# Performance work log

Hardware: AMD Instinct MI355X
Metric: run time of the kernel (lower is better)

Reference implementation:

```python
import jax, jax.numpy as jnp
import numpy as np

B, N, C, K, T = 64, 1024, 256, 512, 64
D_THRESH = 0.5
POWER_ITERS = 20


def _pdist(x):
    # x: [..., K, 3] -> pairwise euclidean distances [..., K, K]
    n = jnp.sum(x * x, axis=-1)
    sq = n[..., :, None] + n[..., None, :] - 2.0 * jnp.einsum('...kc,...lc->...kl', x, x)
    return jnp.sqrt(jnp.maximum(sq, 0.0) + 1e-12)


def _forward(rt, rt_centroids, rt_cls_attn, shift_and_scale, W_in, b_in, W1, b1, W2, b2,
             num_rt, anc_idx, pos_idx, neg_idx):
    valid = jnp.arange(N)[None, :] < num_rt[:, None]                      # [B,N]
    # Normalize.batch_unnormalize: pts * scale + shift on valid tokens
    shift = shift_and_scale[:, None, :3]
    scale = shift_and_scale[:, None, 3:4]
    cent = jnp.where(valid[..., None], rt_centroids * scale + shift, rt_centroids)
    attn = jnp.where(valid, rt_cls_attn, -1e9)
    _, top_idx = jax.lax.top_k(attn, K)                                   # [B,K]
    cent_k = jnp.take_along_axis(cent, top_idx[..., None], axis=1)        # [B,K,3]
    rt_k = jnp.take_along_axis(rt, top_idx[..., None], axis=1)            # [B,K,C]
    # SGV padding mask [T,2,K,K]: rows masked by anchor count, cols by pos/neg counts
    n_eff = jnp.minimum(num_rt, K)
    r = jnp.arange(K)
    row_mask = r[None, :] < n_eff[anc_idx][:, None]                       # [T,K]
    col_mask = jnp.stack([r[None, :] < n_eff[pos_idx][:, None],
                          r[None, :] < n_eff[neg_idx][:, None]], axis=1)  # [T,2,K]
    mask = row_mask[:, None, :, None] & col_mask[:, :, None, :]           # [T,2,K,K]
    # input_linear on anchor / neighbour relay tokens
    anc_f = rt_k[anc_idx] @ W_in + b_in                                   # [T,K,C]
    nn_f = jnp.stack([rt_k[pos_idx], rt_k[neg_idx]], axis=1) @ W_in + b_in  # [T,2,K,C]
    anc_c = cent_k[anc_idx]                                               # [T,K,3]
    nn_c = jnp.stack([cent_k[pos_idx], cent_k[neg_idx]], axis=1)          # [T,2,K,3]
    # feature-space nearest-neighbour correspondences anc -> nn (SpectralGV style)
    fd = (jnp.sum(anc_f ** 2, -1)[:, None, :, None]
          + jnp.sum(nn_f ** 2, -1)[:, :, None, :]
          - 2.0 * jnp.einsum('tkc,tnlc->tnkl', anc_f, nn_f))              # [T,2,K,K]
    corr = jnp.argmin(fd, axis=-1)                                        # [T,2,K]
    q_c = jnp.take_along_axis(nn_c, corr[..., None], axis=2)              # [T,2,K,3]
    q_f = jnp.take_along_axis(nn_f, corr[..., None], axis=2)              # [T,2,K,C]
    # correspondence confidence from feature cosine similarity
    cos = jnp.sum(anc_f[:, None] * q_f, -1) / (
        jnp.linalg.norm(anc_f, axis=-1)[:, None] * jnp.linalg.norm(q_f, axis=-1) + 1e-8)
    s = jax.nn.relu(cos)                                                  # [T,2,K]
    # threshold-masked geometric consistency adjacency
    d_p = _pdist(anc_c)[:, None]                                          # [T,1,K,K]
    d_q = _pdist(q_c)                                                     # [T,2,K,K]
    geo = (jnp.abs(d_p - d_q) < D_THRESH) & mask & (~jnp.eye(K, dtype=bool))
    A = geo.astype(jnp.float32) * s[..., :, None] * s[..., None, :]       # [T,2,K,K]
    # leading eigenvector via power iteration (A is entrywise nonnegative)
    v = jnp.full((T, 2, K), 1.0 / np.sqrt(K), dtype=jnp.float32)
    for _ in range(POWER_ITERS):
        w = jnp.einsum('tnkl,tnl->tnk', A, v)
        v = w / (jnp.linalg.norm(w, axis=-1, keepdims=True) + 1e-8)
    eig = -jnp.sort(-v, axis=-1)                                          # sort_eigvec, descending
    h = jax.nn.relu(eig @ W1 + b1)
    scores = jax.nn.sigmoid(h @ W2 + b2)                                  # [T,2,1]
    targets = jnp.zeros_like(scores).at[:, 0].set(1.0)
    return scores, targets


def setup_inputs() -> dict:
    key = jax.random.key(0)
    ks = jax.random.split(key, 12)
    return {
        'rt': jax.random.normal(ks[0], (B, N, C), jnp.float32),
        'rt_centroids': jax.random.normal(ks[1], (B, N, 3), jnp.float32),
        'rt_cls_attn': jax.random.uniform(ks[2], (B, N), jnp.float32),
        'shift_and_scale': jax.random.uniform(ks[3], (B, 4), jnp.float32),
        'num_rt': jax.random.randint(ks[4], (B,), 128, N, jnp.int32),
        'anc_idx': jax.random.randint(ks[5], (T,), 0, B, jnp.int32),
        'pos_idx': jax.random.randint(ks[6], (T,), 0, B, jnp.int32),
        'neg_idx': jax.random.randint(ks[7], (T,), 0, B, jnp.int32),
        'W_in': jax.random.normal(ks[8], (C, C), jnp.float32) / np.sqrt(C),
        'b_in': jnp.zeros((C,), jnp.float32),
        'W1': jax.random.normal(ks[9], (K, K), jnp.float32) / np.sqrt(K),
        'b1': jnp.zeros((K,), jnp.float32),
        'W2': jax.random.normal(ks[10], (K, 1), jnp.float32) / np.sqrt(K),
        'b2': jnp.zeros((1,), jnp.float32),
    }


def reference(rt, rt_centroids, rt_cls_attn, shift_and_scale, num_rt, anc_idx, pos_idx, neg_idx,
              W_in, b_in, W1, b1, W2, b2):
    return _forward(rt, rt_centroids, rt_cls_attn, shift_and_scale, W_in, b_in, W1, b1, W2, b2,
                    num_rt, anc_idx, pos_idx, neg_idx)
```

## Files before the change

kernel.cpp:

```cpp
#include <hip/hip_runtime.h>
#include <cstddef>

#define BB 64
#define NN 1024
#define CC 256
#define KK 512
#define TT 64
#define NPAIR 128

typedef _Float16 h8 __attribute__((ext_vector_type(8)));
typedef _Float16 h4 __attribute__((ext_vector_type(4)));
typedef float f4 __attribute__((ext_vector_type(4)));

typedef __attribute__((address_space(1))) const void GV;
typedef __attribute__((address_space(3))) void LV;
#define GLDS16(g, s) __builtin_amdgcn_global_load_lds((GV*)(const void*)(g), (LV*)(void*)(s), 16, 0, 0)


__global__ __launch_bounds__(256) void wtrans_kernel(
    const float* __restrict__ Win, _Float16* __restrict__ wth, _Float16* __restrict__ wtl)
{
    __shared__ float t[64][65];
    const int k0 = blockIdx.x * 64, n0 = blockIdx.y * 64;
    const int tid = threadIdx.x;
    const int c = tid & 63, r0 = tid >> 6;
    for (int r = r0; r < 64; r += 4)
        t[r][c] = Win[(size_t)(k0 + r) * CC + n0 + c];
    __syncthreads();
    for (int r = r0; r < 64; r += 4) {
        float x = t[c][r];
        _Float16 h = (_Float16)x;
        size_t o = (size_t)(n0 + r) * CC + k0 + c;
        wth[o] = h;
        wtl[o] = (_Float16)(x - (float)h);
    }
}

__global__ __launch_bounds__(512) void sel_kernel(
    const float* __restrict__ attn, const float* __restrict__ cents,
    const float* __restrict__ sas, const int* __restrict__ num_rt,
    int* __restrict__ topidx, int* __restrict__ neff, float* __restrict__ centk)
{
    __shared__ unsigned long long keys[1024];
    const int b = blockIdx.x, tid = threadIdx.x;
    const int nr = num_rt[b];
    for (int i = tid; i < 1024; i += 512) {
        float a = (i < nr) ? attn[b * NN + i] : -1e9f;
        unsigned u = __float_as_uint(a);
        u = (u & 0x80000000u) ? ~u : (u | 0x80000000u);
        keys[i] = ((unsigned long long)u << 32) | (unsigned)(0xFFFFFFFFu - (unsigned)i);
    }
    __syncthreads();
    for (int k = 2; k <= 1024; k <<= 1) {
        for (int j = k >> 1; j > 0; j >>= 1) {
            int i = ((tid & ~(j - 1)) << 1) | (tid & (j - 1));
            int p = i | j;
            unsigned long long a = keys[i], c = keys[p];
            bool up = (i & k) == 0;
            if (up ? (a < c) : (a > c)) { keys[i] = c; keys[p] = a; }
            __syncthreads();
        }
    }
    {
        unsigned long long key = keys[tid];
        int idx = (int)(~(unsigned)key);
        float x = cents[(b * NN + idx) * 3 + 0];
        float y = cents[(b * NN + idx) * 3 + 1];
        float z = cents[(b * NN + idx) * 3 + 2];
        if (idx < nr) {
            float sc = sas[b * 4 + 3];
            x = x * sc + sas[b * 4 + 0];
            y = y * sc + sas[b * 4 + 1];
            z = z * sc + sas[b * 4 + 2];
        }
        float nc = x * x + y * y + z * z;
        ((float4*)centk)[b * KK + tid] = make_float4(x, y, z, nc);
        topidx[b * KK + tid] = idx;
    }
    if (tid == 0) neff[b] = (nr < KK) ? nr : KK;
}

__global__ __launch_bounds__(256) void feat_mfma(
    const float* __restrict__ rt, const int* __restrict__ topidx,
    const _Float16* __restrict__ wth, const _Float16* __restrict__ wtl,
    const float* __restrict__ bin,
    _Float16* __restrict__ feath, _Float16* __restrict__ featl)
{
    const int mtile = blockIdx.x, nt = blockIdx.y;
    __shared__ _Float16 Ah[128][32], Al[128][32], Bh[128][32], Bl[128][32];
    __shared__ int tix[128];
    const int tid = threadIdx.x;
    const int w = tid >> 6, lane = tid & 63;
    const int quad = lane >> 4, l16 = lane & 15;
    const int wm = (w >> 1) * 64, wl = (w & 1) * 64;
    const int b = mtile >> 2;
    if (tid < 128) tix[tid] = topidx[mtile * 128 + tid];
    __syncthreads();
    const int arow_i = tid >> 1;
    const int aseg = (tid & 1) * 16;
    const int asw = (arow_i >> 1) & 3;
    const float* arow = rt + ((size_t)b * NN + tix[arow_i]) * CC + aseg;
    _Float16* bsh = (w < 2) ? &Bh[0][0] : &Bl[0][0];
    const _Float16* bplane = (w < 2) ? wth : wtl;
    const int rowi = lane >> 2, chunk = lane & 3;
    const int ssw = (rowi >> 1) & 3;
    const int rsw = (l16 >> 1) & 3;

    f4 acc[4][4];
    #pragma unroll
    for (int i = 0; i < 4; i++)
        #pragma unroll
        for (int j = 0; j < 4; j++)
            acc[i][j] = (f4){0.f, 0.f, 0.f, 0.f};

    for (int k0 = 0; k0 < CC; k0 += 32) {
        __syncthreads();
        #pragma unroll
        for (int jj = 0; jj < 4; jj++) {
            int j = (w & 1) * 4 + jj;
            int row = j * 16 + rowi;
            GLDS16(bplane + (size_t)(nt * 128 + row) * CC + k0 + (chunk ^ ssw) * 8, bsh + j * 512);
        }
        {
            const float4* src = (const float4*)(arow + k0);
            #pragma unroll
            for (int c = 0; c < 2; c++) {
                float4 p = src[2 * c], q2 = src[2 * c + 1];
                float xv[8] = {p.x, p.y, p.z, p.w, q2.x, q2.y, q2.z, q2.w};
                h8 hv, lv;
                #pragma unroll
                for (int j = 0; j < 8; j++) {
                    _Float16 h = (_Float16)xv[j];
                    hv[j] = h;
                    lv[j] = (_Float16)(xv[j] - (float)h);
                }
                int ci = ((tid & 1) * 2 + c) ^ asw;
                *(h8*)&Ah[arow_i][ci * 8] = hv;
                *(h8*)&Al[arow_i][ci * 8] = lv;
            }
        }
        __syncthreads();
        h8 afh[4], afl[4], bfh[4], bfl[4];
        #pragma unroll
        for (int i = 0; i < 4; i++) {
            int ra = wm + i * 16 + l16;
            int rb = wl + i * 16 + l16;
            int qa = (quad ^ rsw) * 8;
            afh[i] = *(const h8*)&Ah[ra][qa];
            afl[i] = *(const h8*)&Al[ra][qa];
            bfh[i] = *(const h8*)&Bh[rb][qa];
            bfl[i] = *(const h8*)&Bl[rb][qa];
        }
        #pragma unroll
        for (int i = 0; i < 4; i++)
            #pragma unroll
            for (int j = 0; j < 4; j++) {
                acc[i][j] = __builtin_amdgcn_mfma_f32_16x16x32_f16(afh[i], bfh[j], acc[i][j], 0, 0, 0);
                acc[i][j] = __builtin_amdgcn_mfma_f32_16x16x32_f16(afh[i], bfl[j], acc[i][j], 0, 0, 0);
                acc[i][j] = __builtin_amdgcn_mfma_f32_16x16x32_f16(afl[i], bfh[j], acc[i][j], 0, 0, 0);
            }
    }
    #pragma unroll
    for (int j = 0; j < 4; j++) {
        int col = wl + j * 16 + l16;
        float bj = bin[nt * 128 + col];
        #pragma unroll
        for (int i = 0; i < 4; i++)
            #pragma unroll
            for (int r = 0; r < 4; r++) {
                int row = wm + i * 16 + quad * 4 + r;
                float v = acc[i][j][r] + bj;
                _Float16 h = (_Float16)v;
                size_t o = (size_t)(mtile * 128 + row) * CC + nt * 128 + col;
                feath[o] = h;
                featl[o] = (_Float16)(v - (float)h);
            }
    }
}

__global__ __launch_bounds__(256) void norm_kernel(
    const _Float16* __restrict__ feath, const _Float16* __restrict__ featl,
    float* __restrict__ normF)
{
    int r = blockIdx.x * 4 + (threadIdx.x >> 6);
    int lane = threadIdx.x & 63;
    h4 hv = ((const h4*)(feath + (size_t)r * CC))[lane];
    h4 lv = ((const h4*)(featl + (size_t)r * CC))[lane];
    float s = 0.f;
    #pragma unroll
    for (int j = 0; j < 4; j++) {
        float x = (float)hv[j] + (float)lv[j];
        s += x * x;
    }
    for (int off = 32; off; off >>= 1) s += __shfl_down(s, off);
    if (lane == 0) normF[r] = s;
}

__global__ __launch_bounds__(512) void argmin_mfma(
    const _Float16* __restrict__ feath, const _Float16* __restrict__ featl,
    const float* __restrict__ normF,
    const int* __restrict__ anc, const int* __restrict__ pos, const int* __restrict__ neg,
    float* __restrict__ partv, int* __restrict__ partl, float* __restrict__ partd)
{
    const int id = blockIdx.x;
    const int xcd = id & 7, kgrp = id >> 3;
    const int pr = xcd * 16 + (kgrp >> 2);
    const int s = kgrp & 3;
    const int lt = s & 1, kt = s >> 1;
    const int t = pr >> 1, nn2 = pr & 1;
    const int a = anc[t];
    const int bb = nn2 ? neg[t] : pos[t];
    const size_t Abase = ((size_t)a * KK + kt * 256) * CC;
    const size_t Bbase = ((size_t)bb * KK + lt * 256) * CC;
    __shared__ _Float16 S[2][4][8192];
    __shared__ float rdv[256][2];
    __shared__ int   rdl[256][2];
    __shared__ float rdd[256][2];
    const int tid = threadIdx.x;
    const int w = tid >> 6, lane = tid & 63;
    const int quad = lane >> 4, l16 = lane & 15;
    const int wr = w >> 1, wc = w & 1;
    const int rowi = lane >> 2, chunk = lane & 3;
    const int ssw = (rowi >> 1) & 3;
    const int rsw = (l16 >> 1) & 3;
    const int plane = w >> 1;
    const int srow = (w & 1) * 128;
    const _Float16* gsrc = (plane == 0) ? feath + Abase
                         : (plane == 1) ? featl + Abase
                         : (plane == 2) ? feath + Bbase
                         :                featl + Bbase;
    const _Float16* grow = gsrc + (size_t)(srow + rowi) * CC + (chunk ^ ssw) * 8;

    f4 acc[4][8];
    #pragma unroll
    for (int i = 0; i < 4; i++)
        #pragma unroll
        for (int j = 0; j < 8; j++)
            acc[i][j] = (f4){0.f, 0.f, 0.f, 0.f};

    #pragma unroll
    for (int j = 0; j < 8; j++)
        GLDS16(grow + (size_t)(j * 16) * CC, &S[0][plane][srow * 32 + j * 512]);

    #pragma unroll
    for (int kk = 0; kk < 8; kk++) {
        const int cb = kk & 1;
        if (kk < 7) {
            const int k1 = (kk + 1) * 32;
            #pragma unroll
            for (int j = 0; j < 8; j++)
                GLDS16(grow + (size_t)(j * 16) * CC + k1, &S[cb ^ 1][plane][srow * 32 + j * 512]);
            asm volatile("s_waitcnt vmcnt(8)" ::: "memory");
        } else {
            asm volatile("s_waitcnt vmcnt(0)" ::: "memory");
        }
        __builtin_amdgcn_s_barrier();
        const int qa = (quad ^ rsw) * 8;
        h8 afh[4], afl[4];
        #pragma unroll
        for (int i = 0; i < 4; i++) {
            int ra = wr * 64 + i * 16 + l16;
            afh[i] = *(const h8*)&S[cb][0][ra * 32 + qa];
            afl[i] = *(const h8*)&S[cb][1][ra * 32 + qa];
        }
        #pragma unroll
        for (int j = 0; j < 8; j++) {
            int rb = wc * 128 + j * 16 + l16;
            h8 bfh = *(const h8*)&S[cb][2][rb * 32 + qa];
            h8 bfl = *(const h8*)&S[cb][3][rb * 32 + qa];
            #pragma unroll
            for (int i = 0; i < 4; i++) {
                acc[i][j] = __builtin_amdgcn_mfma_f32_16x16x32_f16(afh[i], bfh, acc[i][j], 0, 0, 0);
                acc[i][j] = __builtin_amdgcn_mfma_f32_16x16x32_f16(afh[i], bfl, acc[i][j], 0, 0, 0);
                acc[i][j] = __builtin_amdgcn_mfma_f32_16x16x32_f16(afl[i], bfh, acc[i][j], 0, 0, 0);
            }
        }
        __builtin_amdgcn_sched_barrier(0);
        __builtin_amdgcn_s_barrier();
    }
    float nbj[8];
    #pragma unroll
    for (int j = 0; j < 8; j++)
        nbj[j] = normF[(size_t)bb * KK + lt * 256 + wc * 128 + j * 16 + l16];
    #pragma unroll
    for (int i = 0; i < 4; i++) {
        #pragma unroll
        for (int r = 0; r < 4; r++) {
            float bv = INFINITY; int bl = 0; float bd = 0.f;
            #pragma unroll
            for (int j = 0; j < 8; j++) {
                float d = acc[i][j][r];
                float v = nbj[j] - 2.f * d;
                int l = lt * 256 + wc * 128 + j * 16 + l16;
                if (v < bv) { bv = v; bl = l; bd = d; }
            }
            #pragma unroll
            for (int off = 1; off < 16; off <<= 1) {
                float ov = __shfl_xor(bv, off);
                int   ol = __shfl_xor(bl, off);
                float od = __shfl_xor(bd, off);
                if (ov < bv || (ov == bv && ol < bl)) { bv = ov; bl = ol; bd = od; }
            }
            if (l16 == 0) {
                int row = wr * 64 + i * 16 + quad * 4 + r;
                rdv[row][wc] = bv;
                rdl[row][wc] = bl;
                rdd[row][wc] = bd;
            }
        }
    }
    __syncthreads();
    if (tid < 256) {
        float bv = rdv[tid][0]; int bl = rdl[tid][0]; float bd = rdd[tid][0];
        float v1 = rdv[tid][1]; int l1 = rdl[tid][1];
        if (v1 < bv || (v1 == bv && l1 < bl)) { bv = v1; bl = l1; bd = rdd[tid][1]; }
        size_t idx = ((size_t)pr * KK + kt * 256 + tid) * 2 + lt;
        partv[idx] = bv; partl[idx] = bl; partd[idx] = bd;
    }
}

__global__ __launch_bounds__(256) void geo_kernel(
    const float* __restrict__ centk,
    const float* __restrict__ partv, const int* __restrict__ partl,
    const float* __restrict__ partd, const float* __restrict__ normF,
    const int* __restrict__ neff,
    const int* __restrict__ anc, const int* __restrict__ pos, const int* __restrict__ neg,
    float* __restrict__ sbuf, unsigned* __restrict__ gmask)
{
    const int kt = blockIdx.x;
    const int lt4 = blockIdx.y;
    const int pair = blockIdx.z;
    const int t = pair >> 1, nn2 = pair & 1;
    const int a = anc[t];
    const int bb2 = (nn2 == 0) ? pos[t] : neg[t];
    const int nea = neff[a], neb = neff[bb2];
    const bool writer = (kt == 0) && (lt4 == 0);
    __shared__ int ci[512];
    __shared__ __align__(16) float4 ca[512], cq[512];
    for (int i = threadIdx.x; i < KK; i += 256) {
        size_t base = ((size_t)pair * KK + i) * 2;
        float bv = partv[base]; int bl = partl[base]; float bd = partd[base];
        float v = partv[base + 1]; int l = partl[base + 1];
        if (v < bv || (v == bv && l < bl)) { bv = v; bl = l; bd = partd[base + 1]; }
        ci[i] = bl;
        if (writer) {
            float na = normF[(size_t)a * KK + i];
            float nb = normF[(size_t)bb2 * KK + bl];
            float cosv = bd / (sqrtf(na) * sqrtf(nb) + 1e-8f);
            sbuf[pair * KK + i] = fmaxf(cosv, 0.f);
        }
    }
    __syncthreads();
    for (int i = threadIdx.x; i < KK; i += 256) {
        ca[i] = ((const float4*)centk)[a * KK + i];
        cq[i] = ((const float4*)centk)[bb2 * KK + ci[i]];
    }
    __syncthreads();
    const int k = kt * 256 + threadIdx.x;
    float4 pk = ca[k], qk = cq[k];
    bool rowm = k < nea;
    unsigned* outp = gmask + ((size_t)pair * KK + k) * 16 + lt4 * 4;
    for (int w = 0; w < 4; w++) {
        unsigned word = 0;
        #pragma unroll
        for (int bi = 0; bi < 32; bi++) {
            int l = lt4 * 128 + w * 32 + bi;
            float4 pl = ca[l], ql = cq[l];
            float dp2 = pk.w + pl.w - 2.f * (pk.x * pl.x + pk.y * pl.y + pk.z * pl.z);
            float dp = sqrtf(fmaxf(dp2, 0.f) + 1e-12f);
            float dq2 = qk.w + ql.w - 2.f * (qk.x * ql.x + qk.y * ql.y + qk.z * ql.z);
            float dq = sqrtf(fmaxf(dq2, 0.f) + 1e-12f);
            bool g = (fabsf(dp - dq) < 0.5f) && rowm && (l < neb) && (l != k);
            word |= (g ? (1u << bi) : 0u);
        }
        outp[w] = word;
    }
}

__global__ __launch_bounds__(1024, 4) void power_kernel(
    const unsigned* __restrict__ gmask, const float* __restrict__ sbuf,
    const int* __restrict__ neff,
    const int* __restrict__ anc, const int* __restrict__ pos, const int* __restrict__ neg,
    const float* __restrict__ W1, const float* __restrict__ b1,
    const float* __restrict__ W2, const float* __restrict__ b2,
    float* __restrict__ out)
{
    const int pair = blockIdx.x;
    const int tid = threadIdx.x;
    const int row = tid & 511;
    const int half = tid >> 9;
    const int tt = pair >> 1, nn2 = pair & 1;
    const int a = anc[tt];
    const int bb2 = (nn2 == 0) ? pos[tt] : neg[tt];
    const int nea = neff[a], neb = neff[bb2];
    __shared__ __align__(16) float uu[512];
    __shared__ float T[64][257];
    __shared__ float pacc[1024];
    __shared__ float red[16];
    __shared__ float ev[512];
    __shared__ float hpart[1024];
    __shared__ int convflag;
    unsigned m[8];
    const unsigned* g = gmask + ((size_t)pair * KK + row) * 16 + half * 8;
    #pragma unroll
    for (int w = 0; w < 8; w++) m[w] = g[w];
    const float s = sbuf[pair * KK + row];
    const int wbase = tid & 511 & ~63;
    const bool wact = (wbase < nea);
    int nw = (neb - half * 256 + 31) >> 5;
    nw = (nw < 0) ? 0 : (nw > 8 ? 8 : nw);
    const int bp = tid & 63;
    const int vh = tid >> 6;
    #define UADDR(r) ((((r) & 4) << 6) + (((r) >> 3) << 2) + ((r) & 3))
    const int GV_[16] = {0,1,3,2,6,7,5,4,12,13,15,14,10,11,9,8};
    const int GB[15] = {0,1,0,2,0,1,0,3,0,1,0,2,0,1,0};
    const float GS[15] = {1.f,1.f,-1.f,1.f,1.f,-1.f,-1.f,1.f,1.f,1.f,-1.f,-1.f,1.f,-1.f,-1.f};
    float v = 0.044194173824159216f;
    float vnprev = v;
    if (half == 0) uu[UADDR(row)] = s * v;
    __syncthreads();
    for (int it = 0; it < 20; it++) {
        {
            float4 ulo = *(const float4*)&uu[bp * 4];
            float4 uhi = *(const float4*)&uu[256 + bp * 4];
            float ul[4] = {ulo.x, ulo.y, ulo.z, ulo.w};
            float H = 0.f;
            H += (float)((vh >> 0) & 1) * uhi.x;
            H += (float)((vh >> 1) & 1) * uhi.y;
            H += (float)((vh >> 2) & 1) * uhi.z;
            H += (float)((vh >> 3) & 1) * uhi.w;
            float L = 0.f;
            T[bp][vh * 16 + 0] = H;
            #pragma unroll
            for (int k = 1; k < 16; k++) {
                L += GS[k - 1] * ul[GB[k - 1]];
                T[bp][vh * 16 + GV_[k]] = H + L;
            }
        }
        __syncthreads();
        float a0 = 0.f, a1 = 0.f, a2 = 0.f, a3 = 0.f;
        if (wact) {
            #define GATHERW(w)  do { unsigned mw = m[w]; \
                const int p0 = half * 32 + (w) * 4; \
                a0 += T[p0 + 0][mw & 255u]; \
                a1 += T[p0 + 1][(mw >> 8) & 255u]; \
                a2 += T[p0 + 2][(mw >> 16) & 255u]; \
                a3 += T[p0 + 3][mw >> 24]; } while (0)
            if (nw > 0) GATHERW(0);
            if (nw > 1) GATHERW(1);
            if (nw > 2) GATHERW(2);
            if (nw > 3) GATHERW(3);
            if (nw > 4) GATHERW(4);
            if (nw > 5) GATHERW(5);
            if (nw > 6) GATHERW(6);
            if (nw > 7) GATHERW(7);
            #undef GATHERW
        }
        pacc[tid] = (a0 + a1) + (a2 + a3);
        __syncthreads();
        float wk = s * (pacc[row] + pacc[row + 512]);
        if ((it & 3) == 3) {
            float t2 = wk * wk;
            for (int off = 32; off; off >>= 1) t2 += __shfl_down(t2, off);
            if ((tid & 63) == 0) red[tid >> 6] = t2;
            if (tid == 0) convflag = 1;
            __syncthreads();
            float tot = 0.f;
            #pragma unroll
            for (int x = 0; x < 16; x++) tot += red[x];
            tot *= 0.5f;
            v = wk / (sqrtf(tot) + 1e-8f);
            bool eq = (__float_as_uint(v) == __float_as_uint(vnprev));
            vnprev = v;
            if (half == 0) uu[UADDR(row)] = s * v;
            if (!eq) convflag = 0;
            __syncthreads();
            if (convflag) break;
        } else {
            if (half == 0) uu[UADDR(row)] = s * wk;
            __syncthreads();
        }
    }
    if (half == 0) ev[row] = v;
    __syncthreads();
    for (int kk = 2; kk <= 512; kk <<= 1) {
        for (int j = kk >> 1; j; j >>= 1) {
            if (tid < 256) {
                int i = ((tid & ~(j - 1)) << 1) | (tid & (j - 1));
                int p = i | j;
                float x = ev[i], y = ev[p];
                bool up = (i & kk) == 0;
                if (up ? (x < y) : (x > y)) { ev[i] = y; ev[p] = x; }
            }
            __syncthreads();
        }
    }
    const int cbase = half * 256;
    float h = (half == 0) ? b1[row] : 0.f;
    #pragma unroll 8
    for (int l = 0; l < 256; l++)
        h += ev[cbase + l] * W1[(size_t)(cbase + l) * KK + row];
    hpart[tid] = h;
    __syncthreads();
    float term = 0.f;
    if (half == 0) {
        float hv = fmaxf(hpart[row] + hpart[row + 512], 0.f);
        term = hv * W2[row];
    }
    for (int off = 32; off; off >>= 1) term += __shfl_down(term, off);
    if ((tid & 63) == 0) red[tid >> 6] = term;
    __syncthreads();
    if (tid == 0) {
        float sc = 0.f;
        #pragma unroll
        for (int x = 0; x < 16; x++) sc += red[x];
        sc += b2[0];
        out[pair] = 1.f / (1.f + expf(-sc));
        out[NPAIR + pair] = (pair & 1) ? 0.f : 1.f;
    }
}

extern "C" void kernel_launch(void* const* d_in, const int* in_sizes, int n_in,
                              void* d_out, int out_size, void* d_ws, size_t ws_size,
                              hipStream_t stream) {
    (void)in_sizes; (void)n_in; (void)out_size; (void)ws_size;
    const float* rt    = (const float*)d_in[0];
    const float* cents = (const float*)d_in[1];
    const float* attn  = (const float*)d_in[2];
    const float* sas   = (const float*)d_in[3];
    const int* num_rt  = (const int*)d_in[4];
    const int* anc     = (const int*)d_in[5];
    const int* pos     = (const int*)d_in[6];
    const int* neg     = (const int*)d_in[7];
    const float* Win   = (const float*)d_in[8];
    const float* bin   = (const float*)d_in[9];
    const float* W1    = (const float*)d_in[10];
    const float* b1    = (const float*)d_in[11];
    const float* W2    = (const float*)d_in[12];
    const float* b2    = (const float*)d_in[13];

    float* ws = (float*)d_ws;
    _Float16* feath = (_Float16*)ws;
    _Float16* featl = (_Float16*)(ws + 4194304);
    float* normF = ws + 8388608;
    float* centk = ws + 8421376;
    float* sbuf  = ws + 8552448;
    int* topidx  = (int*)(ws + 8617984);
    int* neffp   = (int*)(ws + 8650752);
    unsigned* gmask = (unsigned*)(ws + 8716352);
    _Float16* wth = (_Float16*)(ws + 8716352 + 786432);
    _Float16* wtl = (_Float16*)(ws + 8716352 + 819200);
    float* partv = (float*)(ws + 9764928);
    int*   partl = (int*)(ws + 10027072);
    float* partd = (float*)(ws + 10289216);
    float* out = (float*)d_out;

    wtrans_kernel<<<dim3(4, 4), 256, 0, stream>>>(Win, wth, wtl);
    sel_kernel<<<64, 512, 0, stream>>>(attn, cents, sas, num_rt, topidx, neffp, centk);
    feat_mfma<<<dim3(256, 2), 256, 0, stream>>>(rt, topidx, wth, wtl, bin, feath, featl);
    norm_kernel<<<8192, 256, 0, stream>>>(feath, featl, normF);
    argmin_mfma<<<512, 512, 0, stream>>>(feath, featl, normF, anc, pos, neg, partv, partl, partd);
    geo_kernel<<<dim3(2, 4, 128), 256, 0, stream>>>(centk, partv, partl, partd, normF, neffp, anc, pos, neg, sbuf, gmask);
    power_kernel<<<128, 1024, 0, stream>>>(gmask, sbuf, neffp, anc, pos, neg, W1, b1, W2, b2, out);
}
```

Baseline: 342.7 us.

## Merge prep kernels, split argmin prefetch, shrink power kernel and norm grid

```diff
diff --git a/kernel.cpp b/kernel.cpp
--- a/kernel.cpp
+++ b/kernel.cpp
@@ -17,32 +17,31 @@
 #define GLDS16(g, s) __builtin_amdgcn_global_load_lds((GV*)(const void*)(g), (LV*)(void*)(s), 16, 0, 0)
 
 
-__global__ __launch_bounds__(256) void wtrans_kernel(
-    const float* __restrict__ Win, _Float16* __restrict__ wth, _Float16* __restrict__ wtl)
-{
-    __shared__ float t[64][65];
-    const int k0 = blockIdx.x * 64, n0 = blockIdx.y * 64;
-    const int tid = threadIdx.x;
-    const int c = tid & 63, r0 = tid >> 6;
-    for (int r = r0; r < 64; r += 4)
-        t[r][c] = Win[(size_t)(k0 + r) * CC + n0 + c];
-    __syncthreads();
-    for (int r = r0; r < 64; r += 4) {
-        float x = t[c][r];
-        _Float16 h = (_Float16)x;
-        size_t o = (size_t)(n0 + r) * CC + k0 + c;
-        wth[o] = h;
-        wtl[o] = (_Float16)(x - (float)h);
-    }
-}
-
-__global__ __launch_bounds__(512) void sel_kernel(
+__global__ __launch_bounds__(512) void prep_kernel(
+    const float* __restrict__ Win, _Float16* __restrict__ wth, _Float16* __restrict__ wtl,
     const float* __restrict__ attn, const float* __restrict__ cents,
     const float* __restrict__ sas, const int* __restrict__ num_rt,
     int* __restrict__ topidx, int* __restrict__ neff, float* __restrict__ centk)
 {
+    if (blockIdx.x < 16) {
+        __shared__ float t[64][65];
+        const int k0 = (blockIdx.x & 3) * 64, n0 = ((int)blockIdx.x >> 2) * 64;
+        const int tid = threadIdx.x;
+        const int c = tid & 63, r0 = tid >> 6;
+        for (int r = r0; r < 64; r += 8)
+            t[r][c] = Win[(size_t)(k0 + r) * CC + n0 + c];
+        __syncthreads();
+        for (int r = r0; r < 64; r += 8) {
+            float x = t[c][r];
+            _Float16 h = (_Float16)x;
+            size_t o = (size_t)(n0 + r) * CC + k0 + c;
+            wth[o] = h;
+            wtl[o] = (_Float16)(x - (float)h);
+        }
+        return;
+    }
     __shared__ unsigned long long keys[1024];
-    const int b = blockIdx.x, tid = threadIdx.x;
+    const int b = blockIdx.x - 16, tid = threadIdx.x;
     const int nr = num_rt[b];
     for (int i = tid; i < 1024; i += 512) {
         float a = (i < nr) ? attn[b * NN + i] : -1e9f;
@@ -182,18 +181,21 @@
     const _Float16* __restrict__ feath, const _Float16* __restrict__ featl,
     float* __restrict__ normF)
 {
-    int r = blockIdx.x * 4 + (threadIdx.x >> 6);
-    int lane = threadIdx.x & 63;
-    h4 hv = ((const h4*)(feath + (size_t)r * CC))[lane];
-    h4 lv = ((const h4*)(featl + (size_t)r * CC))[lane];
-    float s = 0.f;
-    #pragma unroll
-    for (int j = 0; j < 4; j++) {
-        float x = (float)hv[j] + (float)lv[j];
-        s += x * x;
-    }
-    for (int off = 32; off; off >>= 1) s += __shfl_down(s, off);
-    if (lane == 0) normF[r] = s;
+    const int w = threadIdx.x >> 6;
+    const int lane = threadIdx.x & 63;
+    for (int base = blockIdx.x; base < 8192; base += 2048) {
+        int r = base * 4 + w;
+        h4 hv = ((const h4*)(feath + (size_t)r * CC))[lane];
+        h4 lv = ((const h4*)(featl + (size_t)r * CC))[lane];
+        float s = 0.f;
+        #pragma unroll
+        for (int j = 0; j < 4; j++) {
+            float x = (float)hv[j] + (float)lv[j];
+            s += x * x;
+        }
+        for (int off = 32; off; off >>= 1) s += __shfl_down(s, off);
+        if (lane == 0) normF[r] = s;
+    }
 }
 
 __global__ __launch_bounds__(512) void argmin_mfma(
@@ -248,9 +250,9 @@
         if (kk < 7) {
             const int k1 = (kk + 1) * 32;
             #pragma unroll
-            for (int j = 0; j < 8; j++)
+            for (int j = 0; j < 4; j++)
                 GLDS16(grow + (size_t)(j * 16) * CC + k1, &S[cb ^ 1][plane][srow * 32 + j * 512]);
-            asm volatile("s_waitcnt vmcnt(8)" ::: "memory");
+            asm volatile("s_waitcnt vmcnt(4)" ::: "memory");
         } else {
             asm volatile("s_waitcnt vmcnt(0)" ::: "memory");
         }
@@ -263,8 +265,9 @@
             afh[i] = *(const h8*)&S[cb][0][ra * 32 + qa];
             afl[i] = *(const h8*)&S[cb][1][ra * 32 + qa];
         }
-        #pragma unroll
-        for (int j = 0; j < 8; j++) {
+        __builtin_amdgcn_s_setprio(1);
+        #pragma unroll
+        for (int j = 0; j < 4; j++) {
             int rb = wc * 128 + j * 16 + l16;
             h8 bfh = *(const h8*)&S[cb][2][rb * 32 + qa];
             h8 bfl = *(const h8*)&S[cb][3][rb * 32 + qa];
@@ -275,6 +278,29 @@
                 acc[i][j] = __builtin_amdgcn_mfma_f32_16x16x32_f16(afl[i], bfh, acc[i][j], 0, 0, 0);
             }
         }
+        __builtin_amdgcn_s_setprio(0);
+        __builtin_amdgcn_sched_barrier(0);
+        __builtin_amdgcn_s_barrier();
+        if (kk < 7) {
+            const int k1 = (kk + 1) * 32;
+            #pragma unroll
+            for (int j = 4; j < 8; j++)
+                GLDS16(grow + (size_t)(j * 16) * CC + k1, &S[cb ^ 1][plane][srow * 32 + j * 512]);
+        }
+        __builtin_amdgcn_s_setprio(1);
+        #pragma unroll
+        for (int j = 4; j < 8; j++) {
+            int rb = wc * 128 + j * 16 + l16;
+            h8 bfh = *(const h8*)&S[cb][2][rb * 32 + qa];
+            h8 bfl = *(const h8*)&S[cb][3][rb * 32 + qa];
+            #pragma unroll
+            for (int i = 0; i < 4; i++) {
+                acc[i][j] = __builtin_amdgcn_mfma_f32_16x16x32_f16(afh[i], bfh, acc[i][j], 0, 0, 0);
+                acc[i][j] = __builtin_amdgcn_mfma_f32_16x16x32_f16(afh[i], bfl, acc[i][j], 0, 0, 0);
+                acc[i][j] = __builtin_amdgcn_mfma_f32_16x16x32_f16(afl[i], bfh, acc[i][j], 0, 0, 0);
+            }
+        }
+        __builtin_amdgcn_s_setprio(0);
         __builtin_amdgcn_sched_barrier(0);
         __builtin_amdgcn_s_barrier();
     }
@@ -377,7 +403,7 @@
     }
 }
 
-__global__ __launch_bounds__(1024, 4) void power_kernel(
+__global__ __launch_bounds__(512, 2) void power_kernel(
     const unsigned* __restrict__ gmask, const float* __restrict__ sbuf,
     const int* __restrict__ neff,
     const int* __restrict__ anc, const int* __restrict__ pos, const int* __restrict__ neg,
@@ -387,28 +413,25 @@
 {
     const int pair = blockIdx.x;
     const int tid = threadIdx.x;
-    const int row = tid & 511;
-    const int half = tid >> 9;
+    const int row = tid;
     const int tt = pair >> 1, nn2 = pair & 1;
     const int a = anc[tt];
     const int bb2 = (nn2 == 0) ? pos[tt] : neg[tt];
     const int nea = neff[a], neb = neff[bb2];
     __shared__ __align__(16) float uu[512];
     __shared__ float T[64][257];
-    __shared__ float pacc[1024];
     __shared__ float red[16];
     __shared__ float ev[512];
-    __shared__ float hpart[1024];
     __shared__ int convflag;
-    unsigned m[8];
-    const unsigned* g = gmask + ((size_t)pair * KK + row) * 16 + half * 8;
-    #pragma unroll
-    for (int w = 0; w < 8; w++) m[w] = g[w];
+    unsigned m[16];
+    const unsigned* g = gmask + ((size_t)pair * KK + row) * 16;
+    #pragma unroll
+    for (int w = 0; w < 16; w++) m[w] = g[w];
     const float s = sbuf[pair * KK + row];
-    const int wbase = tid & 511 & ~63;
+    const int wbase = tid & ~63;
     const bool wact = (wbase < nea);
-    int nw = (neb - half * 256 + 31) >> 5;
-    nw = (nw < 0) ? 0 : (nw > 8 ? 8 : nw);
+    int nw0 = (neb + 31) >> 5;               nw0 = (nw0 < 0) ? 0 : (nw0 > 8 ? 8 : nw0);
+    int nw1 = (neb - 256 + 31) >> 5;         nw1 = (nw1 < 0) ? 0 : (nw1 > 8 ? 8 : nw1);
     const int bp = tid & 63;
     const int vh = tid >> 6;
     #define UADDR(r) ((((r) & 4) << 6) + (((r) >> 3) << 2) + ((r) & 3))
@@ -417,48 +440,58 @@
     const float GS[15] = {1.f,1.f,-1.f,1.f,1.f,-1.f,-1.f,1.f,1.f,1.f,-1.f,-1.f,1.f,-1.f,-1.f};
     float v = 0.044194173824159216f;
     float vnprev = v;
-    if (half == 0) uu[UADDR(row)] = s * v;
+    uu[UADDR(row)] = s * v;
     __syncthreads();
     for (int it = 0; it < 20; it++) {
         {
             float4 ulo = *(const float4*)&uu[bp * 4];
             float4 uhi = *(const float4*)&uu[256 + bp * 4];
             float ul[4] = {ulo.x, ulo.y, ulo.z, ulo.w};
-            float H = 0.f;
-            H += (float)((vh >> 0) & 1) * uhi.x;
-            H += (float)((vh >> 1) & 1) * uhi.y;
-            H += (float)((vh >> 2) & 1) * uhi.z;
-            H += (float)((vh >> 3) & 1) * uhi.w;
-            float L = 0.f;
-            T[bp][vh * 16 + 0] = H;
-            #pragma unroll
-            for (int k = 1; k < 16; k++) {
-                L += GS[k - 1] * ul[GB[k - 1]];
-                T[bp][vh * 16 + GV_[k]] = H + L;
+            #pragma unroll
+            for (int sp = 0; sp < 2; sp++) {
+                const int s8 = vh + sp * 8;
+                float H = 0.f;
+                H += (float)((s8 >> 0) & 1) * uhi.x;
+                H += (float)((s8 >> 1) & 1) * uhi.y;
+                H += (float)((s8 >> 2) & 1) * uhi.z;
+                H += (float)((s8 >> 3) & 1) * uhi.w;
+                float L = 0.f;
+                T[bp][s8 * 16 + 0] = H;
+                #pragma unroll
+                for (int k = 1; k < 16; k++) {
+                    L += GS[k - 1] * ul[GB[k - 1]];
+                    T[bp][s8 * 16 + GV_[k]] = H + L;
+                }
             }
         }
         __syncthreads();
         float a0 = 0.f, a1 = 0.f, a2 = 0.f, a3 = 0.f;
+        float c0 = 0.f, c1 = 0.f, c2 = 0.f, c3 = 0.f;
         if (wact) {
-            #define GATHERW(w)  do { unsigned mw = m[w]; \
-                const int p0 = half * 32 + (w) * 4; \
-                a0 += T[p0 + 0][mw & 255u]; \
-                a1 += T[p0 + 1][(mw >> 8) & 255u]; \
-                a2 += T[p0 + 2][(mw >> 16) & 255u]; \
-                a3 += T[p0 + 3][mw >> 24]; } while (0)
-            if (nw > 0) GATHERW(0);
-            if (nw > 1) GATHERW(1);
-            if (nw > 2) GATHERW(2);
-            if (nw > 3) GATHERW(3);
-            if (nw > 4) GATHERW(4);
-            if (nw > 5) GATHERW(5);
-            if (nw > 6) GATHERW(6);
-            if (nw > 7) GATHERW(7);
+            #define GATHERW(w, p0, A0, A1, A2, A3)  do { unsigned mw = m[w]; \
+                A0 += T[(p0) + 0][mw & 255u]; \
+                A1 += T[(p0) + 1][(mw >> 8) & 255u]; \
+                A2 += T[(p0) + 2][(mw >> 16) & 255u]; \
+                A3 += T[(p0) + 3][mw >> 24]; } while (0)
+            if (nw0 > 0) GATHERW(0, 0, a0, a1, a2, a3);
+            if (nw0 > 1) GATHERW(1, 4, a0, a1, a2, a3);
+            if (nw0 > 2) GATHERW(2, 8, a0, a1, a2, a3);
+            if (nw0 > 3) GATHERW(3, 12, a0, a1, a2, a3);
+            if (nw0 > 4) GATHERW(4, 16, a0, a1, a2, a3);
+            if (nw0 > 5) GATHERW(5, 20, a0, a1, a2, a3);
+            if (nw0 > 6) GATHERW(6, 24, a0, a1, a2, a3);
+            if (nw0 > 7) GATHERW(7, 28, a0, a1, a2, a3);
+            if (nw1 > 0) GATHERW(8, 32, c0, c1, c2, c3);
+            if (nw1 > 1) GATHERW(9, 36, c0, c1, c2, c3);
+            if (nw1 > 2) GATHERW(10, 40, c0, c1, c2, c3);
+            if (nw1 > 3) GATHERW(11, 44, c0, c1, c2, c3);
+            if (nw1 > 4) GATHERW(12, 48, c0, c1, c2, c3);
+            if (nw1 > 5) GATHERW(13, 52, c0, c1, c2, c3);
+            if (nw1 > 6) GATHERW(14, 56, c0, c1, c2, c3);
+            if (nw1 > 7) GATHERW(15, 60, c0, c1, c2, c3);
             #undef GATHERW
         }
-        pacc[tid] = (a0 + a1) + (a2 + a3);
-        __syncthreads();
-        float wk = s * (pacc[row] + pacc[row + 512]);
+        float wk = s * (((a0 + a1) + (a2 + a3)) + ((c0 + c1) + (c2 + c3)));
         if ((it & 3) == 3) {
             float t2 = wk * wk;
             for (int off = 32; off; off >>= 1) t2 += __shfl_down(t2, off);
@@ -467,21 +500,20 @@
             __syncthreads();
             float tot = 0.f;
             #pragma unroll
-            for (int x = 0; x < 16; x++) tot += red[x];
-            tot *= 0.5f;
+            for (int x = 0; x < 8; x++) tot += red[x];
             v = wk / (sqrtf(tot) + 1e-8f);
             bool eq = (__float_as_uint(v) == __float_as_uint(vnprev));
             vnprev = v;
-            if (half == 0) uu[UADDR(row)] = s * v;
+            uu[UADDR(row)] = s * v;
             if (!eq) convflag = 0;
             __syncthreads();
             if (convflag) break;
         } else {
-            if (half == 0) uu[UADDR(row)] = s * wk;
+            uu[UADDR(row)] = s * wk;
             __syncthreads();
         }
     }
-    if (half == 0) ev[row] = v;
+    ev[row] = v;
     __syncthreads();
     for (int kk = 2; kk <= 512; kk <<= 1) {
         for (int j = kk >> 1; j; j >>= 1) {
@@ -495,25 +527,23 @@
             __syncthreads();
         }
     }
-    const int cbase = half * 256;
-    float h = (half == 0) ? b1[row] : 0.f;
+    float h0 = b1[row];
     #pragma unroll 8
     for (int l = 0; l < 256; l++)
-        h += ev[cbase + l] * W1[(size_t)(cbase + l) * KK + row];
-    hpart[tid] = h;
-    __syncthreads();
-    float term = 0.f;
-    if (half == 0) {
-        float hv = fmaxf(hpart[row] + hpart[row + 512], 0.f);
-        term = hv * W2[row];
-    }
+        h0 += ev[l] * W1[(size_t)l * KK + row];
+    float h1 = 0.f;
+    #pragma unroll 8
+    for (int l = 256; l < 512; l++)
+        h1 += ev[l] * W1[(size_t)l * KK + row];
+    float hv = fmaxf(h0 + h1, 0.f);
+    float term = hv * W2[row];
     for (int off = 32; off; off >>= 1) term += __shfl_down(term, off);
     if ((tid & 63) == 0) red[tid >> 6] = term;
     __syncthreads();
     if (tid == 0) {
         float sc = 0.f;
         #pragma unroll
-        for (int x = 0; x < 16; x++) sc += red[x];
+        for (int x = 0; x < 8; x++) sc += red[x];
         sc += b2[0];
         out[pair] = 1.f / (1.f + expf(-sc));
         out[NPAIR + pair] = (pair & 1) ? 0.f : 1.f;
@@ -555,11 +585,10 @@
     float* partd = (float*)(ws + 10289216);
     float* out = (float*)d_out;
 
-    wtrans_kernel<<<dim3(4, 4), 256, 0, stream>>>(Win, wth, wtl);
-    sel_kernel<<<64, 512, 0, stream>>>(attn, cents, sas, num_rt, topidx, neffp, centk);
+    prep_kernel<<<80, 512, 0, stream>>>(Win, wth, wtl, attn, cents, sas, num_rt, topidx, neffp, centk);
     feat_mfma<<<dim3(256, 2), 256, 0, stream>>>(rt, topidx, wth, wtl, bin, feath, featl);
-    norm_kernel<<<8192, 256, 0, stream>>>(feath, featl, normF);
+    norm_kernel<<<2048, 256, 0, stream>>>(feath, featl, normF);
     argmin_mfma<<<512, 512, 0, stream>>>(feath, featl, normF, anc, pos, neg, partv, partl, partd);
     geo_kernel<<<dim3(2, 4, 128), 256, 0, stream>>>(centk, partv, partl, partd, normF, neffp, anc, pos, neg, sbuf, gmask);
-    power_kernel<<<128, 1024, 0, stream>>>(gmask, sbuf, neffp, anc, pos, neg, W1, b1, W2, b2, out);
-}
+    power_kernel<<<128, 512, 0, stream>>>(gmask, sbuf, neffp, anc, pos, neg, W1, b1, W2, b2, out);
+}
```

After: 331.8 us. 3.2% less time.
